# Kernel optimization log

Hardware: AMD Instinct MI355X
Metric: run time of the kernel (lower is better)

## Reference

```python
import jax, jax.numpy as jnp
import numpy as np

BS = 128  # block size for gating tiles


def setup_inputs() -> dict:
    key = jax.random.key(0)
    k1, k2, k3 = jax.random.split(key, 3)
    batch, dim_in, dim_out = 1536, 1536, 4608
    X = jax.random.normal(k1, (batch, dim_in), dtype=jnp.float32)
    W = jax.random.normal(k2, (dim_in, dim_out), dtype=jnp.float32)
    G = jax.random.normal(k3, (batch, dim_in // BS, dim_out // BS), dtype=jnp.float32)
    return {"X": X, "W": W, "G": G}


def reference(X, W, G):
    # Block-gated matmul: Y[b, j] = sum_i X[b, i] * W[i, j] * G[b, i//BS, j//BS]
    B, DI = X.shape
    DO = W.shape[1]
    NI, NJ = DI // BS, DO // BS
    Xr = X.reshape(B, NI, BS)               # [B, NI, bs]
    Wr = W.reshape(NI, BS, NJ, BS)          # [NI, bs, NJ, bs]
    # per-input-block partial products gated by G, summed over input blocks
    Y = jnp.einsum('bik,ikjl,bij->bjl', Xr, Wr, G)  # [B, NJ, bs]
    s = Y.sum()
    return s * s
```

## Files before the change

### kernel.cpp

```cpp
#include <hip/hip_runtime.h>


#define B_DIM 1536
#define DI    1536
#define DO    4608
#define NI    12
#define NJ    36
#define GROW  (NI * NJ)
#define BPW   8
#define K2_WAVES  (24 * (B_DIM / BPW))
#define K2_BLOCKS (K2_WAVES / 4)

__global__ __launch_bounds__(256) void wsum_kernel(const float* __restrict__ W,
                                                   float* __restrict__ Wsum) {
    int g    = blockIdx.x * 4 + (threadIdx.x >> 6);
    int lane = threadIdx.x & 63;
    int i = g / 18;
    int w = g - i * 18;
    const float4* p = (const float4*)(W + (size_t)i * DO + (size_t)w * 256);
    float4 v = p[lane];
    float s = (v.x + v.y) + (v.z + v.w);
    #pragma unroll
    for (int off = 16; off > 0; off >>= 1) s += __shfl_xor(s, off, 64);
    if (lane == 0)  Wsum[i * NJ + 2 * w]     = s;
    if (lane == 32) Wsum[i * NJ + 2 * w + 1] = s;
}

__global__ __launch_bounds__(256, 4) void gated_kernel(const float* __restrict__ X,
                                                       const float* __restrict__ G,
                                                       const float* __restrict__ Wsum,
                                                       float* __restrict__ partials) {
    __shared__ float red[4];
    const int t    = threadIdx.x;
    const int w    = __builtin_amdgcn_readfirstlane(t >> 6);
    const int lane = t & 63;
    const int wave = blockIdx.x * 4 + w;
    const int iblk = wave % 24;
    const int brng = wave / 24;
    const int b0   = brng * BPW;
    const int i    = iblk * 64 + lane;
    const int ib   = iblk >> 1;

    float wv[NJ];
    {
        const float4* wsv = (const float4*)(Wsum + (size_t)i * NJ);
        #pragma unroll
        for (int k4 = 0; k4 < 9; ++k4) {
            float4 v = wsv[k4];
            wv[4*k4+0] = v.x; wv[4*k4+1] = v.y;
            wv[4*k4+2] = v.z; wv[4*k4+3] = v.w;
        }
    }
    #pragma unroll
    for (int k = 0; k < NJ; ++k) asm("" : "+v"(wv[k]));

    const float* xp    = X + (size_t)b0 * DI + i;
    const float* gbase = G + (size_t)b0 * GROW + (size_t)ib * NJ;

    float s = 0.f;
    #pragma unroll
    for (int bb = 0; bb < BPW; ++bb) {
        const float4* g4 = (const float4*)(gbase + (size_t)bb * GROW);
        float x = xp[(size_t)bb * DI];
        float d0 = 0.f, d1 = 0.f;
        #pragma unroll
        for (int k4 = 0; k4 < 9; ++k4) {
            float4 gv = g4[k4];
            d0 = fmaf(wv[4*k4+0], gv.x, d0);
            d1 = fmaf(wv[4*k4+1], gv.y, d1);
            d0 = fmaf(wv[4*k4+2], gv.z, d0);
            d1 = fmaf(wv[4*k4+3], gv.w, d1);
        }
        s = fmaf(x, d0 + d1, s);
    }

    #pragma unroll
    for (int off = 1; off < 64; off <<= 1) s += __shfl_xor(s, off, 64);
    if (lane == 0) red[w] = s;
    __syncthreads();
    if (t == 0)
        partials[blockIdx.x] = (red[0] + red[1]) + (red[2] + red[3]);
}

__global__ __launch_bounds__(256) void finish_kernel(const float* __restrict__ partials,
                                                     float* __restrict__ out) {
    __shared__ float red[4];
    const int t = threadIdx.x;
    float s = 0.f;
    for (int e = t; e < K2_BLOCKS; e += 256) s += partials[e];
    #pragma unroll
    for (int off = 1; off < 64; off <<= 1) s += __shfl_xor(s, off, 64);
    const int w = t >> 6, lane = t & 63;
    if (lane == 0) red[w] = s;
    __syncthreads();
    if (t == 0) {
        float tot = (red[0] + red[1]) + (red[2] + red[3]);
        out[0] = tot * tot;
    }
}

extern "C" void kernel_launch(void* const* d_in, const int* in_sizes, int n_in,
                              void* d_out, int out_size, void* d_ws, size_t ws_size,
                              hipStream_t stream) {
    const float* X = (const float*)d_in[0];
    const float* W = (const float*)d_in[1];
    const float* G = (const float*)d_in[2];
    float* out = (float*)d_out;

    float* Wsum     = (float*)d_ws;
    float* partials = Wsum + (size_t)DI * NJ;

    wsum_kernel<<<(DI * 18) / 4, 256, 0, stream>>>(W, Wsum);
    gated_kernel<<<K2_BLOCKS, 256, 0, stream>>>(X, G, Wsum, partials);
    finish_kernel<<<1, 256, 0, stream>>>(partials, out);
}
```

Before: 89.88 us.

## Transpose Wsum layout and stage gate rows in shared memory per block

Wsum is now stored transposed ([NJ][DI]), so each lane's 36 weight-sum loads become coalesced across the wave rather than strided float4 loads per lane. The block cooperatively loads the G rows for its two input blocks and eight batch rows into LDS, and each wave reads its gate values from there instead of issuing redundant uniform global loads. This adds a __syncthreads, and the wsum kernel's stores become scattered.

New measurement: 89.06 us, median of 2. About the same (-0.9%).

```diff
diff --git a/kernel.cpp b/kernel.cpp
--- a/kernel.cpp
+++ b/kernel.cpp
@@ -12,7 +12,7 @@
 #define K2_BLOCKS (K2_WAVES / 4)
 
 __global__ __launch_bounds__(256) void wsum_kernel(const float* __restrict__ W,
-                                                   float* __restrict__ Wsum) {
+                                                   float* __restrict__ WsumT) {
     int g    = blockIdx.x * 4 + (threadIdx.x >> 6);
     int lane = threadIdx.x & 63;
     int i = g / 18;
@@ -22,50 +22,52 @@
     float s = (v.x + v.y) + (v.z + v.w);
     #pragma unroll
     for (int off = 16; off > 0; off >>= 1) s += __shfl_xor(s, off, 64);
-    if (lane == 0)  Wsum[i * NJ + 2 * w]     = s;
-    if (lane == 32) Wsum[i * NJ + 2 * w + 1] = s;
+    if (lane == 0)  WsumT[(size_t)(2 * w)     * DI + i] = s;
+    if (lane == 32) WsumT[(size_t)(2 * w + 1) * DI + i] = s;
 }
 
 __global__ __launch_bounds__(256, 4) void gated_kernel(const float* __restrict__ X,
                                                        const float* __restrict__ G,
-                                                       const float* __restrict__ Wsum,
+                                                       const float* __restrict__ WsumT,
                                                        float* __restrict__ partials) {
+    __shared__ float4 gs4[BPW * 72 / 4];
     __shared__ float red[4];
-    const int t    = threadIdx.x;
-    const int w    = __builtin_amdgcn_readfirstlane(t >> 6);
-    const int lane = t & 63;
-    const int wave = blockIdx.x * 4 + w;
-    const int iblk = wave % 24;
-    const int brng = wave / 24;
-    const int b0   = brng * BPW;
-    const int i    = iblk * 64 + lane;
-    const int ib   = iblk >> 1;
+    float* gs = (float*)gs4;
+
+    const int t     = threadIdx.x;
+    const int w     = t >> 6;
+    const int lane  = t & 63;
+    const int wave0 = blockIdx.x * 4;
+    const int brng  = wave0 / 24;
+    const int a     = (wave0 % 24) >> 2;
+    const int b0    = brng * BPW;
+    const int iblk  = (wave0 % 24) + w;
+    const int i     = iblk * 64 + lane;
+    const int d     = w >> 1;
+
+    for (int e = t; e < BPW * 72; e += 256) {
+        int b = e / 72, r = e - b * 72;
+        gs[e] = G[(size_t)(b0 + b) * GROW + (size_t)(2 * a) * NJ + r];
+    }
 
     float wv[NJ];
-    {
-        const float4* wsv = (const float4*)(Wsum + (size_t)i * NJ);
-        #pragma unroll
-        for (int k4 = 0; k4 < 9; ++k4) {
-            float4 v = wsv[k4];
-            wv[4*k4+0] = v.x; wv[4*k4+1] = v.y;
-            wv[4*k4+2] = v.z; wv[4*k4+3] = v.w;
-        }
-    }
+    #pragma unroll
+    for (int k = 0; k < NJ; ++k) wv[k] = WsumT[(size_t)k * DI + i];
     #pragma unroll
     for (int k = 0; k < NJ; ++k) asm("" : "+v"(wv[k]));
 
-    const float* xp    = X + (size_t)b0 * DI + i;
-    const float* gbase = G + (size_t)b0 * GROW + (size_t)ib * NJ;
+    __syncthreads();
 
+    const float* xp = X + (size_t)b0 * DI + i;
     float s = 0.f;
     #pragma unroll
     for (int bb = 0; bb < BPW; ++bb) {
-        const float4* g4 = (const float4*)(gbase + (size_t)bb * GROW);
         float x = xp[(size_t)bb * DI];
+        const float4* gp = (const float4*)(gs + bb * 72 + d * 36);
         float d0 = 0.f, d1 = 0.f;
         #pragma unroll
         for (int k4 = 0; k4 < 9; ++k4) {
-            float4 gv = g4[k4];
+            float4 gv = gp[k4];
             d0 = fmaf(wv[4*k4+0], gv.x, d0);
             d1 = fmaf(wv[4*k4+1], gv.y, d1);
             d0 = fmaf(wv[4*k4+2], gv.z, d0);
@@ -107,10 +109,10 @@
     const float* G = (const float*)d_in[2];
     float* out = (float*)d_out;
 
-    float* Wsum     = (float*)d_ws;
-    float* partials = Wsum + (size_t)DI * NJ;
+    float* WsumT    = (float*)d_ws;
+    float* partials = WsumT + (size_t)NJ * DI;
 
-    wsum_kernel<<<(DI * 18) / 4, 256, 0, stream>>>(W, Wsum);
-    gated_kernel<<<K2_BLOCKS, 256, 0, stream>>>(X, G, Wsum, partials);
+    wsum_kernel<<<(DI * 18) / 4, 256, 0, stream>>>(W, WsumT);
+    gated_kernel<<<K2_BLOCKS, 256, 0, stream>>>(X, G, WsumT, partials);
     finish_kernel<<<1, 256, 0, stream>>>(partials, out);
 }
```
